# Kernel tuning notes

Hardware: AMD Instinct MI355X
Metric: run time of the kernel (lower is better)

The kernel has to match this reference:

```python
import jax, jax.numpy as jnp
import numpy as np

N_NODES = 100000
N_EDGES = 1600000
D_IN = 64
D_OUT = 64
BN_EPS = 1e-5


def setup_inputs() -> dict:
    key = jax.random.key(0)
    k_x, k_e, k_w, k_b = jax.random.split(key, 4)
    x = jax.random.normal(k_x, (N_NODES, D_IN), dtype=jnp.float32)
    edge_index = jax.random.randint(k_e, (2, N_EDGES), 0, N_NODES, dtype=jnp.int64)
    # GCNConv linear weight (glorot-ish) and bias
    W = jax.random.normal(k_w, (D_IN, D_OUT), dtype=jnp.float32) / np.sqrt(D_IN)
    b = jnp.zeros((D_OUT,), dtype=jnp.float32)
    # BatchNorm affine params (init: weight=1, bias=0)
    bn_weight = jnp.ones((D_OUT,), dtype=jnp.float32)
    bn_bias = jnp.zeros((D_OUT,), dtype=jnp.float32)
    return {"x": x, "edge_index": edge_index, "num_nodes": N_NODES,
            "W": W, "b": b, "bn_weight": bn_weight, "bn_bias": bn_bias}


def reference(x, edge_index, num_nodes, W, b, bn_weight, bn_bias):
    # --- self-loop handling (layer_idx=1) ---
    # _add_custom_self_loops removes existing self-loops and adds 1 per node;
    # PyG gcn_norm's add_remaining_self_loops then keeps exactly one unit-weight
    # self-loop per node. Equivalent (jit-friendly, static shapes): zero-weight
    # any existing self-loop edges and append one self-loop per node.
    src, dst = edge_index[0], edge_index[1]
    ew = (src != dst).astype(x.dtype)                      # [E]
    loop = jnp.arange(num_nodes, dtype=src.dtype)
    src_a = jnp.concatenate([src, loop])                   # [E+N]
    dst_a = jnp.concatenate([dst, loop])
    ew_a = jnp.concatenate([ew, jnp.ones((num_nodes,), x.dtype)])

    # --- symmetric GCN normalization: D^-1/2 A D^-1/2 ---
    deg = jax.ops.segment_sum(ew_a, dst_a, num_segments=num_nodes)  # [N]
    dinv = jnp.where(deg > 0, jax.lax.rsqrt(deg), 0.0)
    norm = dinv[src_a] * ew_a * dinv[dst_a]                # [E+N]

    # --- transform then aggregate (gather -> scatter-add) ---
    h = x @ W                                              # [N, D_OUT]
    msgs = h[src_a] * norm[:, None]                        # [E+N, D_OUT]
    out = jax.ops.segment_sum(msgs, dst_a, num_segments=num_nodes) + b

    # --- BatchNorm (training: batch stats, biased var) + ReLU ---
    mean = jnp.mean(out, axis=0)
    var = jnp.mean(jnp.square(out - mean), axis=0)
    y = (out - mean) * jax.lax.rsqrt(var + BN_EPS) * bn_weight + bn_bias
    return jax.nn.relu(y)
```

## Files before the change

kernel.cpp:

```cpp
#include <hip/hip_runtime.h>

#define NN 100000
#define D 64
#define BN_EPS 1e-5f


__global__ void k_zero(int* cnt, float* sums8, int n) {
    int i = blockIdx.x * blockDim.x + threadIdx.x;
    if (i < n) cnt[i] = 0;
    if (i < 1152) sums8[i] = 0.0f;
}

__global__ void k_count4(const int* __restrict__ src, const int* __restrict__ dst,
                         int* cnt, int E) {
    int t = blockIdx.x * blockDim.x + threadIdx.x;
    int e0 = t * 4;
    if (e0 >= E) return;
    if (e0 + 4 <= E) {
        int4 s4 = *(const int4*)(src + e0);
        int4 d4 = *(const int4*)(dst + e0);
        if (s4.x != d4.x) atomicAdd(&cnt[d4.x], 1);
        if (s4.y != d4.y) atomicAdd(&cnt[d4.y], 1);
        if (s4.z != d4.z) atomicAdd(&cnt[d4.z], 1);
        if (s4.w != d4.w) atomicAdd(&cnt[d4.w], 1);
    } else {
        for (int e = e0; e < E; ++e) {
            int s = src[e], d = dst[e];
            if (s != d) atomicAdd(&cnt[d], 1);
        }
    }
}

__global__ void k_dinv_i(const int* __restrict__ cnt, float* dinv, int n) {
    int i = blockIdx.x * blockDim.x + threadIdx.x;
    if (i < n) dinv[i] = rsqrtf((float)cnt[i] + 1.0f);
}

__global__ __launch_bounds__(1024) void k_scanA(const int* __restrict__ cnt,
                                                int* __restrict__ row_ptr,
                                                int* __restrict__ bsum, int n) {
    __shared__ int sm[1024];
    int tid = threadIdx.x;
    int i = blockIdx.x * 1024 + tid;
    int v = (i < n) ? cnt[i] : 0;
    int xv = v;
    sm[tid] = xv;
    __syncthreads();
    for (int off = 1; off < 1024; off <<= 1) {
        int t = (tid >= off) ? sm[tid - off] : 0;
        __syncthreads();
        xv += t;
        sm[tid] = xv;
        __syncthreads();
    }
    if (i < n) row_ptr[i] = xv - v;
    if (tid == 1023) bsum[blockIdx.x] = xv;
}

__global__ void k_scanB(int* bsum, int nb) {
    __shared__ int sm[128];
    int tid = threadIdx.x;
    int v = (tid < nb) ? bsum[tid] : 0;
    int xv = v;
    sm[tid] = xv;
    __syncthreads();
    for (int off = 1; off < 128; off <<= 1) {
        int t = (tid >= off) ? sm[tid - off] : 0;
        __syncthreads();
        xv += t;
        sm[tid] = xv;
        __syncthreads();
    }
    if (tid < nb) bsum[tid] = xv - v;
}

__global__ void k_scanC(int* __restrict__ row_ptr, int* __restrict__ cursor,
                        const int* __restrict__ bsum, int n) {
    int i = blockIdx.x * blockDim.x + threadIdx.x;
    if (i < n) {
        int r = row_ptr[i] + bsum[i >> 10];
        row_ptr[i] = r;
        cursor[i] = r;
    }
}

__global__ void k_place8(const int* __restrict__ src, const int* __restrict__ dst,
                         int* cursor, int* __restrict__ srcid, int E) {
    int t = blockIdx.x * blockDim.x + threadIdx.x;
    int e0 = t * 8;
    if (e0 >= E) return;
    if (e0 + 8 <= E) {
        int4 sa = *(const int4*)(src + e0);
        int4 sb = *(const int4*)(src + e0 + 4);
        int4 da = *(const int4*)(dst + e0);
        int4 db = *(const int4*)(dst + e0 + 4);
        if (sa.x != da.x) srcid[atomicAdd(&cursor[da.x], 1)] = sa.x;
        if (sa.y != da.y) srcid[atomicAdd(&cursor[da.y], 1)] = sa.y;
        if (sa.z != da.z) srcid[atomicAdd(&cursor[da.z], 1)] = sa.z;
        if (sa.w != da.w) srcid[atomicAdd(&cursor[da.w], 1)] = sa.w;
        if (sb.x != db.x) srcid[atomicAdd(&cursor[db.x], 1)] = sb.x;
        if (sb.y != db.y) srcid[atomicAdd(&cursor[db.y], 1)] = sb.y;
        if (sb.z != db.z) srcid[atomicAdd(&cursor[db.z], 1)] = sb.z;
        if (sb.w != db.w) srcid[atomicAdd(&cursor[db.w], 1)] = sb.w;
    } else {
        for (int e = e0; e < E; ++e) {
            int s = src[e], d = dst[e];
            if (s != d) srcid[atomicAdd(&cursor[d], 1)] = s;
        }
    }
}

__global__ __launch_bounds__(256) void k_gather_gemm_stats(
        const int* __restrict__ row_ptr, const int* __restrict__ cnt,
        const int* __restrict__ srcid, const float* __restrict__ x,
        const float* __restrict__ dinv, const float* __restrict__ W,
        float* __restrict__ out, float* sums8, int n) {
    __shared__ float Ws[64 * 64];
    int tid = threadIdx.x;
    for (int i = tid; i < 64 * 64; i += 256) Ws[i] = W[i];
    __syncthreads();
    int wave = tid >> 6, lane = tid & 63;
    float s = 0.0f, sq = 0.0f;
    for (int d = blockIdx.x * 4 + wave; d < n; d += gridDim.x * 4) {
        int base = row_ptr[d];
        int c = cnt[d];
        float did = dinv[d];
        float acc = x[(size_t)d * D + lane] * did * did;
        int j = 0;
        for (; j + 8 <= c; j += 8) {
            int si[8];
            float wv[8], xv[8];
#pragma unroll
            for (int u = 0; u < 8; ++u) si[u] = srcid[base + j + u];
#pragma unroll
            for (int u = 0; u < 8; ++u) wv[u] = dinv[si[u]] * did;
#pragma unroll
            for (int u = 0; u < 8; ++u) xv[u] = x[(size_t)si[u] * D + lane];
#pragma unroll
            for (int u = 0; u < 8; ++u) acc += xv[u] * wv[u];
        }
        for (; j < c; ++j) {
            int si = srcid[base + j];
            acc += x[(size_t)si * D + lane] * (dinv[si] * did);
        }
        float o = 0.0f;
#pragma unroll
        for (int k = 0; k < 64; ++k) {
            o += __shfl(acc, k) * Ws[k * 64 + lane];
        }
        out[(size_t)d * D + lane] = o;
        s += o;
        sq += o * o;
    }
    __shared__ float ls[4][64], lq[4][64];
    ls[wave][lane] = s;
    lq[wave][lane] = sq;
    __syncthreads();
    if (wave == 0) {
        float ts = ls[0][lane] + ls[1][lane] + ls[2][lane] + ls[3][lane];
        float tq = lq[0][lane] + lq[1][lane] + lq[2][lane] + lq[3][lane];
        float* slot = sums8 + (size_t)(blockIdx.x & 7) * 128;
        atomicAdd(&slot[lane], ts);
        atomicAdd(&slot[64 + lane], tq);
    }
}

__global__ void k_finalize(float* sums8) {
    int i = threadIdx.x;
    float s = 0.0f;
#pragma unroll
    for (int j = 0; j < 8; ++j) s += sums8[j * 128 + i];
    sums8[1024 + i] = s;
}

__global__ void k_bn_apply(float* out, const float* __restrict__ sums,
                           const float* __restrict__ bnw, const float* __restrict__ bnb,
                           int n) {
    int i = blockIdx.x * blockDim.x + threadIdx.x;
    int total = n * (D / 4);
    if (i >= total) return;
    int c0 = (i * 4) & 63;
    const float invn = 1.0f / (float)NN;
    float4 v = ((const float4*)out)[i];
    float r[4] = {v.x, v.y, v.z, v.w};
#pragma unroll
    for (int j = 0; j < 4; ++j) {
        int c = c0 + j;
        float mean = sums[c] * invn;
        float var = sums[64 + c] * invn - mean * mean;
        if (var < 0.0f) var = 0.0f;
        float scale = bnw[c] * rsqrtf(var + BN_EPS);
        float y = (r[j] - mean) * scale + bnb[c];
        r[j] = y > 0.0f ? y : 0.0f;
    }
    float4 o = {r[0], r[1], r[2], r[3]};
    ((float4*)out)[i] = o;
}


__global__ void k_deg_init(float* deg, int n) {
    int i = blockIdx.x * blockDim.x + threadIdx.x;
    if (i < n) deg[i] = 1.0f;
}

__global__ void k_deg_edges(const int* __restrict__ src, const int* __restrict__ dst,
                            float* deg, int E) {
    int e = blockIdx.x * blockDim.x + threadIdx.x;
    if (e < E) {
        int s = src[e], d = dst[e];
        if (s != d) atomicAdd(&deg[d], 1.0f);
    }
}

__global__ void k_dinv_f(float* deg, int n) {
    int i = blockIdx.x * blockDim.x + threadIdx.x;
    if (i < n) deg[i] = rsqrtf(deg[i]);
}

__global__ void k_agg_init(const float* __restrict__ x, const float* __restrict__ dinv,
                           float* __restrict__ out, int n) {
    int i = blockIdx.x * blockDim.x + threadIdx.x;
    int total = n * (D / 4);
    if (i >= total) return;
    int row = i >> 4;
    float di = dinv[row];
    float sc = di * di;
    float4 v = ((const float4*)x)[i];
    v.x *= sc; v.y *= sc; v.z *= sc; v.w *= sc;
    ((float4*)out)[i] = v;
}

__global__ __launch_bounds__(256) void k_scatter(const int* __restrict__ src,
                                                 const int* __restrict__ dst,
                                                 const float* __restrict__ x,
                                                 const float* __restrict__ dinv,
                                                 float* out, int E) {
    int gw = (int)((blockIdx.x * blockDim.x + threadIdx.x) >> 6);
    int lane = threadIdx.x & 63;
    if (gw >= E) return;
    int s = src[gw], d = dst[gw];
    if (s == d) return;
    float w = dinv[s] * dinv[d];
    atomicAdd(&out[(size_t)d * D + lane], x[(size_t)s * D + lane] * w);
}

__global__ void k_zero_stats(float* sums) {
    int i = threadIdx.x;
    if (i < 128) sums[i] = 0.0f;
}

__global__ __launch_bounds__(256) void k_gemm_stats(float* __restrict__ out,
                                                    const float* __restrict__ W,
                                                    float* sums, int n) {
    __shared__ float Ws[64 * 64];
    int tid = threadIdx.x;
    for (int i = tid; i < 64 * 64; i += 256) Ws[i] = W[i];
    __syncthreads();
    int wave = tid >> 6, lane = tid & 63;
    float s = 0.0f, sq = 0.0f;
    for (int row = blockIdx.x * 4 + wave; row < n; row += gridDim.x * 4) {
        float xv = out[(size_t)row * D + lane];
        float acc = 0.0f;
#pragma unroll
        for (int k = 0; k < 64; ++k) {
            acc += __shfl(xv, k) * Ws[k * 64 + lane];
        }
        out[(size_t)row * D + lane] = acc;
        s += acc;
        sq += acc * acc;
    }
    __shared__ float ls[4][64], lq[4][64];
    ls[wave][lane] = s;
    lq[wave][lane] = sq;
    __syncthreads();
    if (wave == 0) {
        float ts = ls[0][lane] + ls[1][lane] + ls[2][lane] + ls[3][lane];
        float tq = lq[0][lane] + lq[1][lane] + lq[2][lane] + lq[3][lane];
        atomicAdd(&sums[lane], ts);
        atomicAdd(&sums[64 + lane], tq);
    }
}

extern "C" void kernel_launch(void* const* d_in, const int* in_sizes, int n_in,
                              void* d_out, int out_size, void* d_ws, size_t ws_size,
                              hipStream_t stream) {
    const float* x = (const float*)d_in[0];
    const int* ei = (const int*)d_in[1];
    const float* W = (const float*)d_in[3];
    const float* bnw = (const float*)d_in[5];
    const float* bnb = (const float*)d_in[6];
    float* out = (float*)d_out;

    const int n = in_sizes[0] / D;
    const int E = in_sizes[1] / 2;
    const int* src = ei;
    const int* dst = ei + E;

    const size_t need = ((size_t)4 * n + (size_t)E + 1408) * 4;

    if (ws_size >= need) {
        int* cnt = (int*)d_ws;
        int* row_ptr = cnt + n;
        int* cursor = row_ptr + n;
        float* dinv = (float*)(cursor + n);
        int* srcid = (int*)(dinv + n);
        int* bsum = srcid + E;
        float* sums8 = (float*)(bsum + 128);
        float* sums = sums8 + 1024;

        const int nb = (n + 1023) / 1024;

        k_zero<<<(n + 255) / 256, 256, 0, stream>>>(cnt, sums8, n);
        k_count4<<<((E + 3) / 4 + 255) / 256, 256, 0, stream>>>(src, dst, cnt, E);
        k_dinv_i<<<(n + 255) / 256, 256, 0, stream>>>(cnt, dinv, n);
        k_scanA<<<nb, 1024, 0, stream>>>(cnt, row_ptr, bsum, n);
        k_scanB<<<1, 128, 0, stream>>>(bsum, nb);
        k_scanC<<<(n + 255) / 256, 256, 0, stream>>>(row_ptr, cursor, bsum, n);
        k_place8<<<((E + 7) / 8 + 255) / 256, 256, 0, stream>>>(src, dst, cursor, srcid, E);

        k_gather_gemm_stats<<<4096, 256, 0, stream>>>(row_ptr, cnt, srcid, x, dinv, W,
                                                      out, sums8, n);
        k_finalize<<<1, 128, 0, stream>>>(sums8);
        k_bn_apply<<<(n * (D / 4) + 255) / 256, 256, 0, stream>>>(out, sums, bnw, bnb, n);
    } else {
        float* dinv = (float*)d_ws;
        float* sums = dinv + n;
        k_deg_init<<<(n + 255) / 256, 256, 0, stream>>>(dinv, n);
        k_deg_edges<<<(E + 255) / 256, 256, 0, stream>>>(src, dst, dinv, E);
        k_dinv_f<<<(n + 255) / 256, 256, 0, stream>>>(dinv, n);
        k_agg_init<<<(n * (D / 4) + 255) / 256, 256, 0, stream>>>(x, dinv, out, n);
        k_scatter<<<(E + 3) / 4, 256, 0, stream>>>(src, dst, x, dinv, out, E);
        k_zero_stats<<<1, 128, 0, stream>>>(sums);
        k_gemm_stats<<<1024, 256, 0, stream>>>(out, W, sums, n);
        k_bn_apply<<<(n * (D / 4) + 255) / 256, 256, 0, stream>>>(out, sums, bnw, bnb, n);
    }
}
```

Baseline: 397.4 us.

## Gather neighbor features from a prescaled bf16 copy of x

Adds a pass that prescales each row of x by its dinv and stores it as bf16, and a new gather+GEMM kernel that reads these 2-byte features during neighbor aggregation. The goal is to roughly halve the random-gather memory traffic, which dominates the aggregation, and to drop the per-edge dinv multiply. It costs an extra full pass over x plus bf16 rounding error in the messages, and it removes the non-CSR fallback path.

```diff
diff --git a/kernel.cpp b/kernel.cpp
--- a/kernel.cpp
+++ b/kernel.cpp
@@ -3,6 +3,18 @@
 #define NN 100000
 #define D 64
 #define BN_EPS 1e-5f
+
+typedef unsigned short ushort_t;
+typedef unsigned int uint_t;
+
+__device__ __forceinline__ ushort_t f2b_rne(float f) {
+    uint_t u = __float_as_uint(f);
+    uint_t r = (u + 0x7FFFu + ((u >> 16) & 1u)) >> 16;
+    return (ushort_t)r;
+}
+__device__ __forceinline__ float b2f(ushort_t u) {
+    return __uint_as_float(((uint_t)u) << 16);
+}
 
 
 __global__ void k_zero(int* cnt, float* sums8, int n) {
@@ -34,6 +46,22 @@
 __global__ void k_dinv_i(const int* __restrict__ cnt, float* dinv, int n) {
     int i = blockIdx.x * blockDim.x + threadIdx.x;
     if (i < n) dinv[i] = rsqrtf((float)cnt[i] + 1.0f);
+}
+
+__global__ void k_xb(const float* __restrict__ x, const float* __restrict__ dinv,
+                     ushort_t* __restrict__ xb, int n) {
+    int i = blockIdx.x * blockDim.x + threadIdx.x;
+    int total = n * (D / 4);
+    if (i >= total) return;
+    int row = i >> 4;
+    float di = dinv[row];
+    float4 v = ((const float4*)x)[i];
+    ushort4 o;
+    o.x = f2b_rne(v.x * di);
+    o.y = f2b_rne(v.y * di);
+    o.z = f2b_rne(v.z * di);
+    o.w = f2b_rne(v.w * di);
+    ((ushort4*)xb)[i] = o;
 }
 
 __global__ __launch_bounds__(1024) void k_scanA(const int* __restrict__ cnt,
@@ -110,6 +138,61 @@
     }
 }
 
+__global__ __launch_bounds__(256) void k_gather_gemm_stats_bf16(
+        const int* __restrict__ row_ptr, const int* __restrict__ cnt,
+        const int* __restrict__ srcid, const float* __restrict__ x,
+        const ushort_t* __restrict__ xb, const float* __restrict__ dinv,
+        const float* __restrict__ W, float* __restrict__ out, float* sums8, int n) {
+    __shared__ float Ws[64 * 64];
+    int tid = threadIdx.x;
+    for (int i = tid; i < 64 * 64; i += 256) Ws[i] = W[i];
+    __syncthreads();
+    int wave = tid >> 6, lane = tid & 63;
+    float s = 0.0f, sq = 0.0f;
+    for (int d = blockIdx.x * 4 + wave; d < n; d += gridDim.x * 4) {
+        int base = row_ptr[d];
+        int c = cnt[d];
+        float did = dinv[d];
+        float self = x[(size_t)d * D + lane];
+        float acc = 0.0f;
+        int j = 0;
+        for (; j + 8 <= c; j += 8) {
+            int si[8];
+            float xv[8];
+#pragma unroll
+            for (int u = 0; u < 8; ++u) si[u] = srcid[base + j + u];
+#pragma unroll
+            for (int u = 0; u < 8; ++u) xv[u] = b2f(xb[(size_t)si[u] * D + lane]);
+#pragma unroll
+            for (int u = 0; u < 8; ++u) acc += xv[u];
+        }
+        for (; j < c; ++j) {
+            int si = srcid[base + j];
+            acc += b2f(xb[(size_t)si * D + lane]);
+        }
+        float agg = did * (did * self + acc);
+        float o = 0.0f;
+#pragma unroll
+        for (int k = 0; k < 64; ++k) {
+            o += __shfl(agg, k) * Ws[k * 64 + lane];
+        }
+        out[(size_t)d * D + lane] = o;
+        s += o;
+        sq += o * o;
+    }
+    __shared__ float ls[4][64], lq[4][64];
+    ls[wave][lane] = s;
+    lq[wave][lane] = sq;
+    __syncthreads();
+    if (wave == 0) {
+        float ts = ls[0][lane] + ls[1][lane] + ls[2][lane] + ls[3][lane];
+        float tq = lq[0][lane] + lq[1][lane] + lq[2][lane] + lq[3][lane];
+        float* slot = sums8 + (size_t)(blockIdx.x & 7) * 128;
+        atomicAdd(&slot[lane], ts);
+        atomicAdd(&slot[64 + lane], tq);
+    }
+}
+
 __global__ __launch_bounds__(256) void k_gather_gemm_stats(
         const int* __restrict__ row_ptr, const int* __restrict__ cnt,
         const int* __restrict__ srcid, const float* __restrict__ x,
@@ -197,90 +280,6 @@
     ((float4*)out)[i] = o;
 }
 
-
-__global__ void k_deg_init(float* deg, int n) {
-    int i = blockIdx.x * blockDim.x + threadIdx.x;
-    if (i < n) deg[i] = 1.0f;
-}
-
-__global__ void k_deg_edges(const int* __restrict__ src, const int* __restrict__ dst,
-                            float* deg, int E) {
-    int e = blockIdx.x * blockDim.x + threadIdx.x;
-    if (e < E) {
-        int s = src[e], d = dst[e];
-        if (s != d) atomicAdd(&deg[d], 1.0f);
-    }
-}
-
-__global__ void k_dinv_f(float* deg, int n) {
-    int i = blockIdx.x * blockDim.x + threadIdx.x;
-    if (i < n) deg[i] = rsqrtf(deg[i]);
-}
-
-__global__ void k_agg_init(const float* __restrict__ x, const float* __restrict__ dinv,
-                           float* __restrict__ out, int n) {
-    int i = blockIdx.x * blockDim.x + threadIdx.x;
-    int total = n * (D / 4);
-    if (i >= total) return;
-    int row = i >> 4;
-    float di = dinv[row];
-    float sc = di * di;
-    float4 v = ((const float4*)x)[i];
-    v.x *= sc; v.y *= sc; v.z *= sc; v.w *= sc;
-    ((float4*)out)[i] = v;
-}
-
-__global__ __launch_bounds__(256) void k_scatter(const int* __restrict__ src,
-                                                 const int* __restrict__ dst,
-                                                 const float* __restrict__ x,
-                                                 const float* __restrict__ dinv,
-                                                 float* out, int E) {
-    int gw = (int)((blockIdx.x * blockDim.x + threadIdx.x) >> 6);
-    int lane = threadIdx.x & 63;
-    if (gw >= E) return;
-    int s = src[gw], d = dst[gw];
-    if (s == d) return;
-    float w = dinv[s] * dinv[d];
-    atomicAdd(&out[(size_t)d * D + lane], x[(size_t)s * D + lane] * w);
-}
-
-__global__ void k_zero_stats(float* sums) {
-    int i = threadIdx.x;
-    if (i < 128) sums[i] = 0.0f;
-}
-
-__global__ __launch_bounds__(256) void k_gemm_stats(float* __restrict__ out,
-                                                    const float* __restrict__ W,
-                                                    float* sums, int n) {
-    __shared__ float Ws[64 * 64];
-    int tid = threadIdx.x;
-    for (int i = tid; i < 64 * 64; i += 256) Ws[i] = W[i];
-    __syncthreads();
-    int wave = tid >> 6, lane = tid & 63;
-    float s = 0.0f, sq = 0.0f;
-    for (int row = blockIdx.x * 4 + wave; row < n; row += gridDim.x * 4) {
-        float xv = out[(size_t)row * D + lane];
-        float acc = 0.0f;
-#pragma unroll
-        for (int k = 0; k < 64; ++k) {
-            acc += __shfl(xv, k) * Ws[k * 64 + lane];
-        }
-        out[(size_t)row * D + lane] = acc;
-        s += acc;
-        sq += acc * acc;
-    }
-    __shared__ float ls[4][64], lq[4][64];
-    ls[wave][lane] = s;
-    lq[wave][lane] = sq;
-    __syncthreads();
-    if (wave == 0) {
-        float ts = ls[0][lane] + ls[1][lane] + ls[2][lane] + ls[3][lane];
-        float tq = lq[0][lane] + lq[1][lane] + lq[2][lane] + lq[3][lane];
-        atomicAdd(&sums[lane], ts);
-        atomicAdd(&sums[64 + lane], tq);
-    }
-}
-
 extern "C" void kernel_launch(void* const* d_in, const int* in_sizes, int n_in,
                               void* d_out, int out_size, void* d_ws, size_t ws_size,
                               hipStream_t stream) {
@@ -296,9 +295,11 @@
     const int* src = ei;
     const int* dst = ei + E;
 
-    const size_t need = ((size_t)4 * n + (size_t)E + 1408) * 4;
-
-    if (ws_size >= need) {
+    const size_t base_words = (size_t)4 * n + (size_t)E + 1280;
+    const size_t need_csr = base_words * 4;
+    const size_t need_bf16 = need_csr + 16 + (size_t)n * D * 2;
+
+    if (ws_size >= need_csr) {
         int* cnt = (int*)d_ws;
         int* row_ptr = cnt + n;
         int* cursor = row_ptr + n;
@@ -307,6 +308,8 @@
         int* bsum = srcid + E;
         float* sums8 = (float*)(bsum + 128);
         float* sums = sums8 + 1024;
+        size_t off = ((size_t)(sums8 + 1152 - (float*)d_ws) * 4 + 15) & ~(size_t)15;
+        ushort_t* xb = (ushort_t*)((char*)d_ws + off);
 
         const int nb = (n + 1023) / 1024;
 
@@ -318,20 +321,15 @@
         k_scanC<<<(n + 255) / 256, 256, 0, stream>>>(row_ptr, cursor, bsum, n);
         k_place8<<<((E + 7) / 8 + 255) / 256, 256, 0, stream>>>(src, dst, cursor, srcid, E);
 
-        k_gather_gemm_stats<<<4096, 256, 0, stream>>>(row_ptr, cnt, srcid, x, dinv, W,
-                                                      out, sums8, n);
+        if (ws_size >= need_bf16) {
+            k_xb<<<(n * (D / 4) + 255) / 256, 256, 0, stream>>>(x, dinv, xb, n);
+            k_gather_gemm_stats_bf16<<<4096, 256, 0, stream>>>(row_ptr, cnt, srcid, x, xb,
+                                                               dinv, W, out, sums8, n);
+        } else {
+            k_gather_gemm_stats<<<4096, 256, 0, stream>>>(row_ptr, cnt, srcid, x, dinv, W,
+                                                          out, sums8, n);
+        }
         k_finalize<<<1, 128, 0, stream>>>(sums8);
         k_bn_apply<<<(n * (D / 4) + 255) / 256, 256, 0, stream>>>(out, sums, bnw, bnb, n);
-    } else {
-        float* dinv = (float*)d_ws;
-        float* sums = dinv + n;
-        k_deg_init<<<(n + 255) / 256, 256, 0, stream>>>(dinv, n);
-        k_deg_edges<<<(E + 255) / 256, 256, 0, stream>>>(src, dst, dinv, E);
-        k_dinv_f<<<(n + 255) / 256, 256, 0, stream>>>(dinv, n);
-        k_agg_init<<<(n * (D / 4) + 255) / 256, 256, 0, stream>>>(x, dinv, out, n);
-        k_scatter<<<(E + 3) / 4, 256, 0, stream>>>(src, dst, x, dinv, out, E);
-        k_zero_stats<<<1, 128, 0, stream>>>(sums);
-        k_gemm_stats<<<1024, 256, 0, stream>>>(out, W, sums, n);
-        k_bn_apply<<<(n * (D / 4) + 255) / 256, 256, 0, stream>>>(out, sums, bnw, bnb, n);
-    }
-}
+    }
+}
```

Measured after the change: 399.2 us. No clear change (+0.4%).
